# Optimization experiments

Hardware: AMD Instinct MI355X
Metric: run time of the kernel (lower is better)

Reference implementation:

```python
import jax, jax.numpy as jnp
import numpy as np

BN_EPS = 1e-5
LEAKY_SLOPE = 0.01

def setup_inputs() -> dict:
    key = jax.random.key(0)
    ks = jax.random.split(key, 8)
    B, N, C, D = 8, 2048, 128, 32  # batch, points, inchannels, outchannels
    s = 0.05
    return {
        "x": jax.random.normal(ks[0], (B, N, C), dtype=jnp.float32),
        "Wq": jax.random.normal(ks[1], (D, C), dtype=jnp.float32) * s,
        "Wk": jax.random.normal(ks[2], (D, C), dtype=jnp.float32) * s,
        "Wv": jax.random.normal(ks[3], (C, C), dtype=jnp.float32) * s,
        "Wp": jax.random.normal(ks[4], (C, C), dtype=jnp.float32) * s,
        "bn_gamma": jnp.ones((C,), dtype=jnp.float32),
        "bn_beta": jnp.zeros((C,), dtype=jnp.float32),
        "bn_mean": jax.random.normal(ks[5], (C,), dtype=jnp.float32) * 0.01,
        "bn_var": jnp.abs(jax.random.normal(ks[6], (C,), dtype=jnp.float32)) * 0.1 + 0.9,
    }

def reference(x, Wq, Wk, Wv, Wp, bn_gamma, bn_beta, bn_mean, bn_var):
    # x: [B, N, C]; 1x1 Conv1d == per-point linear map
    q = jnp.einsum('bnc,dc->bnd', x, Wq)          # [B, N, D]
    k = jnp.einsum('bnc,dc->bnd', x, Wk)          # [B, N, D]
    v = jnp.einsum('bnc,oc->bno', x, Wv)          # [B, N, C]
    energy = jnp.einsum('bnd,bmd->bnm', q, k)     # [B, Nq, Nk]
    # offset-attention: softmax over the QUERY axis (dim=1), then L1-renorm over keys
    attn = jax.nn.softmax(energy, axis=1)
    attn = attn / (1e-9 + attn.sum(axis=-1, keepdims=True))
    x_r = jnp.einsum('bnm,bmc->bnc', attn, v)     # [B, N, C]
    # project(x - x_r): 1x1 conv + BatchNorm (eval, running stats) + LeakyReLU; dropout p=0
    d = x - x_r
    y = jnp.einsum('bnc,oc->bno', d, Wp)
    y = (y - bn_mean) * (bn_gamma / jnp.sqrt(bn_var + BN_EPS)) + bn_beta
    y = jnp.where(y >= 0, y, LEAKY_SLOPE * y)
    return y + x
```

## Files before the change

### kernel.cpp

```cpp
#include <hip/hip_runtime.h>
#include <stdint.h>

#define BB 8
#define NN 2048
#define CC 128
#define DD 32
#define LOG2E 1.44269504088896340736f

typedef __attribute__((ext_vector_type(8))) short short8;
typedef __attribute__((ext_vector_type(4))) short short4v;
typedef __attribute__((ext_vector_type(4))) float f32x4;

#define MFMA(a,b,c) __builtin_amdgcn_mfma_f32_16x16x32_bf16(a,b,c,0,0,0)

__device__ __forceinline__ short f2b(float f){
  uint32_t u = __float_as_uint(f);
  uint32_t r = (u + 0x7fffu + ((u >> 16) & 1u)) >> 16;
  return (short)r;
}
__device__ __forceinline__ float b2f(short s){
  uint32_t u = ((uint32_t)(uint16_t)s) << 16;
  return __uint_as_float(u);
}

__global__ void k_pack(const float* __restrict__ Wq, const float* __restrict__ Wk,
                       const float* __restrict__ Wv, const float* __restrict__ Wp,
                       const float* __restrict__ g, const float* __restrict__ bt,
                       const float* __restrict__ mu, const float* __restrict__ vr,
                       short* __restrict__ wqkv, short* __restrict__ wp,
                       float* __restrict__ scale, float* __restrict__ shift){
  int i = blockIdx.x*256 + threadIdx.x;
  if (i < 192*128){
    int r = i >> 7, c = i & 127;
    float w = (r < 32) ? Wq[r*128+c] : (r < 64) ? Wk[(r-32)*128+c] : Wv[(r-64)*128+c];
    wqkv[i] = f2b(w);
  }
  if (i < 128*128) wp[i] = f2b(Wp[i]);
  if (i < 128){
    float s = g[i] * rsqrtf(vr[i] + 1e-5f);
    scale[i] = s;
    shift[i] = bt[i] - mu[i]*s;
  }
}

__global__ __launch_bounds__(256,4) void k_qkv(const float* __restrict__ x, const short* __restrict__ wqkv,
    short* __restrict__ qb, short* __restrict__ kb, short* __restrict__ vt){
  const int tid = threadIdx.x;
  const int wv = tid >> 6, l = tid & 63, lrow = l & 15, lg = l >> 4;
  const int r0 = blockIdx.x*16;
  const int base = wv*3;
  const float* xr = x + (long)(r0 + lrow)*CC;
  short8 a[4];
  #pragma unroll
  for (int ks=0; ks<4; ks++){
    f32x4 u0 = *(const f32x4*)(xr + ks*32 + lg*8);
    f32x4 u1 = *(const f32x4*)(xr + ks*32 + lg*8 + 4);
    short8 t;
    #pragma unroll
    for (int j=0;j<4;j++){ t[j] = f2b(u0[j]); t[4+j] = f2b(u1[j]); }
    a[ks] = t;
  }
  f32x4 acc[3];
  #pragma unroll
  for (int i=0;i<3;i++) acc[i] = f32x4{0.f,0.f,0.f,0.f};
  #pragma unroll
  for (int of=0; of<3; of++){
    #pragma unroll
    for (int ks=0; ks<4; ks++){
      short8 bfr = *(const short8*)(wqkv + ((base+of)*16 + lrow)*CC + ks*32 + lg*8);
      acc[of] = MFMA(a[ks], bfr, acc[of]);
    }
  }
  const int b = r0 / NN, nin = r0 % NN;
  #pragma unroll
  for (int of=0; of<3; of++){
    const int oo = base + of;
    const int o = oo*16 + lrow;
    if (oo < 2){
      #pragma unroll
      for (int rr=0; rr<4; rr++) qb[(long)(r0 + lg*4 + rr)*DD + o] = f2b(acc[of][rr]*LOG2E);
    } else if (oo < 4){
      #pragma unroll
      for (int rr=0; rr<4; rr++) kb[(long)(r0 + lg*4 + rr)*DD + (o-32)] = f2b(acc[of][rr]);
    } else {
      short4v s;
      #pragma unroll
      for (int rr=0; rr<4; rr++) s[rr] = f2b(acc[of][rr]);
      *(short4v*)(vt + (long)(b*CC + (o-64))*NN + nin + lg*4) = s;
    }
  }
}

__global__ __launch_bounds__(256,4) void k_colsum(const short* __restrict__ qb, const short* __restrict__ kb,
                                                  float* __restrict__ csum){
  const int tid = threadIdx.x;
  const int wv = tid >> 6, l = tid & 63, lrow = l & 15, lg = l >> 4;
  const int bq = blockIdx.x & 31;
  const int b = bq >> 2, q = bq & 3;
  const int m0 = (blockIdx.x >> 5)*64 + wv*16;
  short8 afr = *(const short8*)(kb + (long)(b*NN + m0 + lrow)*DD + lg*8);
  const short* qbase = qb + (long)b*NN*DD;
  float sum[4] = {0.f,0.f,0.f,0.f};
  f32x4 z = {0.f,0.f,0.f,0.f};
  const int nbeg = q*512, nend = nbeg + 512;
  #pragma unroll 4
  for (int n0=nbeg; n0<nend; n0+=16){
    short8 bfr = *(const short8*)(qbase + (long)(n0 + lrow)*DD + lg*8);
    f32x4 e = MFMA(afr, bfr, z);
    #pragma unroll
    for (int r=0;r<4;r++) sum[r] += exp2f(e[r]);
  }
  #pragma unroll
  for (int mask=1; mask<16; mask<<=1){
    #pragma unroll
    for (int r=0;r<4;r++) sum[r] += __shfl_xor(sum[r], mask);
  }
  if (lrow == 0){
    #pragma unroll
    for (int r=0;r<4;r++) csum[q*(BB*NN) + b*NN + m0 + lg*4 + r] = sum[r];
  }
}

__global__ __launch_bounds__(256,4) void k_attn(const short* __restrict__ qb,
    const short* __restrict__ kb, const short* __restrict__ vt, const float* __restrict__ csum,
    short* __restrict__ accPb, float* __restrict__ Lp){
  __shared__ __align__(16) short lds[17408];
  const int tid = threadIdx.x;
  const int wv = tid >> 6, l = tid & 63, lrow = l & 15, lg = l >> 4;
  const int bq = blockIdx.x & 31;
  const int b = bq >> 2;
  const int quarter = bq & 3;
  const int rt = blockIdx.x >> 5;
  const int n0 = rt*64 + wv*16;
  short8 qfr = *(const short8*)(qb + (long)(b*NN + n0 + lrow)*DD + lg*8);
  const short* kbb = kb + (long)b*NN*DD;
  const short* vtb = vt + (long)b*CC*NN;
  float* sinvl = (float*)(lds + 16384);

  const int mbase = quarter*512;
  {
    const float* c0 = csum + b*NN + mbase;
    #pragma unroll
    for (int i=tid; i<512; i+=256){
      float s = c0[i] + c0[i + BB*NN] + c0[i + 2*BB*NN] + c0[i + 3*BB*NN];
      sinvl[i] = __builtin_amdgcn_rcpf(s);
    }
  }

  f32x4 acc[8];
  #pragma unroll
  for (int i=0;i<8;i++) acc[i] = f32x4{0.f,0.f,0.f,0.f};
  float L[4] = {0.f,0.f,0.f,0.f};

  short8 sv[4]; short8 sk[2];
  const int cr = tid >> 1, hf = tid & 1;

  auto loadT = [&](int m0){
    const short* s = vtb + (long)cr*NN + m0 + hf*32;
    sv[0] = *(const short8*)(s);
    sv[1] = *(const short8*)(s+8);
    sv[2] = *(const short8*)(s+16);
    sv[3] = *(const short8*)(s+24);
    if (tid < 128){
      const short* s2 = kbb + (long)(m0 + cr)*DD + hf*16;
      sk[0] = *(const short8*)(s2);
      sk[1] = *(const short8*)(s2+8);
    }
  };
  auto storeT = [&](){
    short* vt_t = lds;
    *(short8*)(vt_t + cr*72 + hf*32 + 0)  = sv[0];
    *(short8*)(vt_t + cr*72 + hf*32 + 8)  = sv[1];
    *(short8*)(vt_t + cr*72 + hf*32 + 16) = sv[2];
    *(short8*)(vt_t + cr*72 + hf*32 + 24) = sv[3];
    if (tid < 128){
      short* kb_t = vt_t + 9216;
      *(short8*)(kb_t + cr*40 + hf*16 + 0) = sk[0];
      *(short8*)(kb_t + cr*40 + hf*16 + 8) = sk[1];
    }
  };

  loadT(mbase);
  storeT();
  __syncthreads();

  short* pl = lds + 11776 + wv*1152;
  f32x4 z = {0.f,0.f,0.f,0.f};
  for (int it=0; it<8; it++){
    const int m0 = mbase + it*64;
    if (it < 7) loadT(m0 + 64);
    short* vt_t = lds;
    short* kb_t = lds + 9216;
    float p[16];
    #pragma unroll
    for (int mt=0; mt<4; mt++){
      short8 bfr = *(short8*)(kb_t + (mt*16 + lrow)*40 + lg*8);
      f32x4 e = MFMA(qfr, bfr, z);
      float si = sinvl[it*64 + mt*16 + lrow];
      #pragma unroll
      for (int r=0;r<4;r++) p[mt*4+r] = exp2f(e[r]) * si;
    }
    #pragma unroll
    for (int r=0;r<4;r++) L[r] += (p[r] + p[4+r]) + (p[8+r] + p[12+r]);
    #pragma unroll
    for (int mt=0; mt<4; mt++){
      #pragma unroll
      for (int r=0;r<4;r++)
        pl[(lg*4+r)*72 + mt*16 + lrow] = f2b(p[mt*4+r]);
    }
    __builtin_amdgcn_s_setprio(1);
    #pragma unroll
    for (int ks=0; ks<2; ks++){
      short8 pa = *(short8*)(pl + lrow*72 + ks*32 + lg*8);
      #pragma unroll
      for (int cf=0; cf<8; cf++){
        short8 vb_ = *(short8*)(vt_t + (cf*16 + lrow)*72 + ks*32 + lg*8);
        acc[cf] = MFMA(pa, vb_, acc[cf]);
      }
    }
    __builtin_amdgcn_s_setprio(0);
    __syncthreads();
    if (it < 7){
      storeT();
      __syncthreads();
    }
  }

  #pragma unroll
  for (int mask=1; mask<16; mask<<=1){
    #pragma unroll
    for (int r=0;r<4;r++) L[r] += __shfl_xor(L[r], mask);
  }

  const long tile = (long)((b*32 + rt)*4 + quarter);
  short* aP = accPb + tile*64*128;
  #pragma unroll
  for (int cf=0; cf<8; cf++){
    #pragma unroll
    for (int r=0;r<4;r++)
      aP[(wv*16 + lg*4 + r)*128 + cf*16 + lrow] = f2b(acc[cf][r]);
  }
  if (lrow == 0){
    #pragma unroll
    for (int r=0;r<4;r++) Lp[tile*64 + wv*16 + lg*4 + r] = L[r];
  }
}

__global__ __launch_bounds__(256,4) void k_fin(const float* __restrict__ x, const short* __restrict__ accPb,
    const float* __restrict__ Lp, const short* __restrict__ wp, const float* __restrict__ scale,
    const float* __restrict__ shift, float* __restrict__ out){
  __shared__ __align__(16) short dl[16*136];
  __shared__ float linv_s[16];
  const int tid = threadIdx.x;
  const int wv = tid >> 6, l = tid & 63, lrow = l & 15, lg = l >> 4;
  const int b = blockIdx.x >> 7;
  const int rt = blockIdx.x & 127;
  const int nb = rt*16;
  const long tileIdx = (long)(b*32 + (rt>>2))*4;
  const int rowoff = (rt&3)*16;

  if (tid < 16){
    float Ls = Lp[(tileIdx+0)*64 + rowoff + tid] + Lp[(tileIdx+1)*64 + rowoff + tid]
             + Lp[(tileIdx+2)*64 + rowoff + tid] + Lp[(tileIdx+3)*64 + rowoff + tid];
    linv_s[tid] = __builtin_amdgcn_rcpf(1e-9f + Ls);
  }

  const int row_l = tid >> 4;
  const int c0 = (tid & 15)*8;
  float a[8];
  #pragma unroll
  for (int j=0;j<8;j++) a[j] = 0.f;
  #pragma unroll
  for (int p=0;p<4;p++){
    short8 v = *(const short8*)(accPb + (tileIdx+p)*64*128 + (rowoff+row_l)*128 + c0);
    #pragma unroll
    for (int j=0;j<8;j++) a[j] += b2f(v[j]);
  }
  const float* xr = x + ((long)(b*NN + nb + row_l))*CC + c0;
  f32x4 x0 = *(const f32x4*)(xr);
  f32x4 x1 = *(const f32x4*)(xr + 4);
  __syncthreads();
  {
    const float li = linv_s[row_l];
    short4v d0, d1;
    #pragma unroll
    for (int j=0;j<4;j++){
      d0[j] = f2b(x0[j] - a[j]*li);
      d1[j] = f2b(x1[j] - a[4+j]*li);
    }
    *(short4v*)(dl + row_l*136 + c0) = d0;
    *(short4v*)(dl + row_l*136 + c0 + 4) = d1;
  }
  __syncthreads();

  f32x4 yac[2];
  yac[0] = f32x4{0.f,0.f,0.f,0.f};
  yac[1] = f32x4{0.f,0.f,0.f,0.f};
  #pragma unroll
  for (int ks=0; ks<4; ks++){
    short8 da = *(short8*)(dl + lrow*136 + ks*32 + lg*8);
    #pragma unroll
    for (int of=0; of<2; of++){
      short8 wfr = *(const short8*)(wp + ((wv*2+of)*16 + lrow)*CC + ks*32 + lg*8);
      yac[of] = MFMA(da, wfr, yac[of]);
    }
  }
  float* ob = out + ((long)(b*NN + nb))*CC;
  const float* xb = x + ((long)(b*NN + nb))*CC;
  #pragma unroll
  for (int of=0; of<2; of++){
    const int o = (wv*2+of)*16 + lrow;
    const float sc = scale[o], sh = shift[o];
    #pragma unroll
    for (int r=0;r<4;r++){
      float y = yac[of][r]*sc + sh;
      y = (y >= 0.f) ? y : 0.01f*y;
      ob[(lg*4+r)*CC + o] = y + xb[(lg*4+r)*CC + o];
    }
  }
}

__global__ __launch_bounds__(256) void k_attn_mono(const float* __restrict__ x, const short* __restrict__ qb,
    const short* __restrict__ kb, const short* __restrict__ vt, const float* __restrict__ csum,
    const short* __restrict__ wp, const float* __restrict__ scale, const float* __restrict__ shift,
    float* __restrict__ out){
  __shared__ __align__(16) short lds[28160];
  const int tid = threadIdx.x;
  const int wv = tid >> 6, l = tid & 63, lrow = l & 15, lg = l >> 4;
  const int b = blockIdx.x >> 5;
  const int n0 = (blockIdx.x & 31)*64 + wv*16;
  short8 qfr = *(const short8*)(qb + (long)(b*NN + n0 + lrow)*DD + lg*8);
  const short* kbb = kb + (long)b*NN*DD;
  const short* vtb = vt + (long)b*CC*NN;
  const float* c0 = csum + b*NN;

  f32x4 acc[8];
  #pragma unroll
  for (int i=0;i<8;i++) acc[i] = f32x4{0.f,0.f,0.f,0.f};
  float L[4] = {0.f,0.f,0.f,0.f};
  short8 sv[4]; short8 sk[2];
  const int cr = tid >> 1, hf = tid & 1;
  auto loadT = [&](int m0){
    const short* s = vtb + (long)cr*NN + m0 + hf*32;
    sv[0] = *(const short8*)(s); sv[1] = *(const short8*)(s+8);
    sv[2] = *(const short8*)(s+16); sv[3] = *(const short8*)(s+24);
    if (tid < 128){
      const short* s2 = kbb + (long)(m0 + cr)*DD + hf*16;
      sk[0] = *(const short8*)(s2); sk[1] = *(const short8*)(s2+8);
    }
  };
  auto storeT = [&](int buf){
    short* vt_t = lds + buf*11776;
    *(short8*)(vt_t + cr*72 + hf*32 + 0)  = sv[0];
    *(short8*)(vt_t + cr*72 + hf*32 + 8)  = sv[1];
    *(short8*)(vt_t + cr*72 + hf*32 + 16) = sv[2];
    *(short8*)(vt_t + cr*72 + hf*32 + 24) = sv[3];
    if (tid < 128){
      short* kb_t = vt_t + 9216;
      *(short8*)(kb_t + cr*40 + hf*16 + 0) = sk[0];
      *(short8*)(kb_t + cr*40 + hf*16 + 8) = sk[1];
    }
  };
  loadT(0); storeT(0); __syncthreads();
  short* pl = lds + 23552 + wv*1152;
  f32x4 z = {0.f,0.f,0.f,0.f};
  for (int it=0; it<32; it++){
    const int m0 = it*64;
    const int cur = it & 1;
    if (it < 31) loadT(m0 + 64);
    short* vt_t = lds + cur*11776;
    short* kb_t = vt_t + 9216;
    float p[16];
    #pragma unroll
    for (int mt=0; mt<4; mt++){
      short8 bfr = *(short8*)(kb_t + (mt*16 + lrow)*40 + lg*8);
      f32x4 e = MFMA(qfr, bfr, z);
      const int m = m0 + mt*16 + lrow;
      float si = __builtin_amdgcn_rcpf(c0[m] + c0[m+BB*NN] + c0[m+2*BB*NN] + c0[m+3*BB*NN]);
      #pragma unroll
      for (int r=0;r<4;r++) p[mt*4+r] = exp2f(e[r]) * si;
    }
    #pragma unroll
    for (int r=0;r<4;r++) L[r] += (p[r] + p[4+r]) + (p[8+r] + p[12+r]);
    #pragma unroll
    for (int mt=0; mt<4; mt++){
      #pragma unroll
      for (int r=0;r<4;r++)
        pl[(lg*4+r)*72 + mt*16 + lrow] = f2b(p[mt*4+r]);
    }
    #pragma unroll
    for (int ks=0; ks<2; ks++){
      short8 pa = *(short8*)(pl + lrow*72 + ks*32 + lg*8);
      #pragma unroll
      for (int cf=0; cf<8; cf++){
        short8 vb_ = *(short8*)(vt_t + (cf*16 + lrow)*72 + ks*32 + lg*8);
        acc[cf] = MFMA(pa, vb_, acc[cf]);
      }
    }
    if (it < 31) storeT((it+1) & 1);
    __syncthreads();
  }
  #pragma unroll
  for (int mask=1; mask<16; mask<<=1){
    #pragma unroll
    for (int r=0;r<4;r++) L[r] += __shfl_xor(L[r], mask);
  }
  float linv[4];
  #pragma unroll
  for (int r=0;r<4;r++) linv[r] = __builtin_amdgcn_rcpf(1e-9f + L[r]);
  const float* xbb = x + (long)(b*NN + n0)*CC;
  float xv[32];
  short* dl = lds + wv*2176;
  #pragma unroll
  for (int cf=0; cf<8; cf++){
    #pragma unroll
    for (int r=0;r<4;r++){
      float xx = xbb[(lg*4+r)*CC + cf*16 + lrow];
      xv[cf*4+r] = xx;
      dl[(lg*4+r)*136 + cf*16 + lrow] = f2b(xx - acc[cf][r]*linv[r]);
    }
  }
  f32x4 yac[8];
  #pragma unroll
  for (int i=0;i<8;i++) yac[i] = f32x4{0.f,0.f,0.f,0.f};
  #pragma unroll
  for (int ks=0; ks<4; ks++){
    short8 da = *(short8*)(dl + lrow*136 + ks*32 + lg*8);
    #pragma unroll
    for (int of=0; of<8; of++){
      short8 wfr = *(const short8*)(wp + (of*16 + lrow)*CC + ks*32 + lg*8);
      yac[of] = MFMA(da, wfr, yac[of]);
    }
  }
  float* ob = out + (long)(b*NN + n0)*CC;
  #pragma unroll
  for (int of=0; of<8; of++){
    const int o = of*16 + lrow;
    const float sc = scale[o], sh = shift[o];
    #pragma unroll
    for (int r=0;r<4;r++){
      float y = yac[of][r]*sc + sh;
      y = (y >= 0.f) ? y : 0.01f*y;
      ob[(lg*4+r)*CC + o] = y + xv[of*4+r];
    }
  }
}

extern "C" void kernel_launch(void* const* d_in, const int* in_sizes, int n_in,
                              void* d_out, int out_size, void* d_ws, size_t ws_size,
                              hipStream_t stream) {
  const float* x  = (const float*)d_in[0];
  const float* Wq = (const float*)d_in[1];
  const float* Wk = (const float*)d_in[2];
  const float* Wv = (const float*)d_in[3];
  const float* Wp = (const float*)d_in[4];
  const float* g  = (const float*)d_in[5];
  const float* bt = (const float*)d_in[6];
  const float* mu = (const float*)d_in[7];
  const float* vr = (const float*)d_in[8];
  float* out = (float*)d_out;

  char* ws = (char*)d_ws;
  short* wqkv  = (short*)(ws + 0);
  short* wp    = (short*)(ws + 49152);
  float* scale = (float*)(ws + 81920);
  float* shift = (float*)(ws + 82432);
  short* qb    = (short*)(ws + 98304);
  short* kb    = (short*)(ws + 1146880);
  short* vt    = (short*)(ws + 2195456);
  float* csum  = (float*)(ws + 6389760);
  float* Lp    = (float*)(ws + 6651904);
  short* accPb = (short*)(ws + 6914048);
  const size_t need_split = 6914048 + 16777216;

  k_pack<<<96, 256, 0, stream>>>(Wq, Wk, Wv, Wp, g, bt, mu, vr, wqkv, wp, scale, shift);
  k_qkv<<<1024, 256, 0, stream>>>(x, wqkv, qb, kb, vt);
  k_colsum<<<1024, 256, 0, stream>>>(qb, kb, csum);
  if (ws_size >= need_split){
    k_attn<<<1024, 256, 0, stream>>>(qb, kb, vt, csum, accPb, Lp);
    k_fin<<<1024, 256, 0, stream>>>(x, accPb, Lp, wp, scale, shift, out);
  } else {
    k_attn_mono<<<256, 256, 0, stream>>>(x, qb, kb, vt, csum, wp, scale, shift, out);
  }
}
```

Baseline: 131.2 us.

## Split attention key dimension across waves and drop weight packing kernel

The attention kernel now gives each wave a 16-key slice, and every wave handles all 64 query rows. Each wave computes transposed energy with K as the A operand, so the probabilities feed straight into 16x16x16 MFMAs against V without a round trip through LDS. Partial accumulators from the four waves are then reduced through LDS in bf16 before being written out. This drops the per-wave P staging, but it raises register pressure (launch bounds go to 2 blocks per SIMD) and adds an extra bf16 rounding step. Separately, the k_pack kernel is removed, with the weights converted to bf16 and the BN scale/shift computed inline in k_qkv and k_fin. The mono fallback path is also deleted.

```diff
diff --git a/kernel.cpp b/kernel.cpp
--- a/kernel.cpp
+++ b/kernel.cpp
@@ -13,6 +13,17 @@
 
 #define MFMA(a,b,c) __builtin_amdgcn_mfma_f32_16x16x32_bf16(a,b,c,0,0,0)
 
+__device__ __forceinline__ f32x4 MFMA16(short4v a, short4v b, f32x4 c){
+#if __has_builtin(__builtin_amdgcn_mfma_f32_16x16x16bf16_1k)
+  return __builtin_amdgcn_mfma_f32_16x16x16bf16_1k(a, b, c, 0, 0, 0);
+#else
+  f32x4 d;
+  asm volatile("s_nop 1\n\tv_mfma_f32_16x16x16_bf16 %0, %1, %2, %3\n\ts_nop 4"
+               : "=&v"(d) : "v"(a), "v"(b), "v"(c));
+  return d;
+#endif
+}
+
 __device__ __forceinline__ short f2b(float f){
   uint32_t u = __float_as_uint(f);
   uint32_t r = (u + 0x7fffu + ((u >> 16) & 1u)) >> 16;
@@ -23,27 +34,8 @@
   return __uint_as_float(u);
 }
 
-__global__ void k_pack(const float* __restrict__ Wq, const float* __restrict__ Wk,
-                       const float* __restrict__ Wv, const float* __restrict__ Wp,
-                       const float* __restrict__ g, const float* __restrict__ bt,
-                       const float* __restrict__ mu, const float* __restrict__ vr,
-                       short* __restrict__ wqkv, short* __restrict__ wp,
-                       float* __restrict__ scale, float* __restrict__ shift){
-  int i = blockIdx.x*256 + threadIdx.x;
-  if (i < 192*128){
-    int r = i >> 7, c = i & 127;
-    float w = (r < 32) ? Wq[r*128+c] : (r < 64) ? Wk[(r-32)*128+c] : Wv[(r-64)*128+c];
-    wqkv[i] = f2b(w);
-  }
-  if (i < 128*128) wp[i] = f2b(Wp[i]);
-  if (i < 128){
-    float s = g[i] * rsqrtf(vr[i] + 1e-5f);
-    scale[i] = s;
-    shift[i] = bt[i] - mu[i]*s;
-  }
-}
-
-__global__ __launch_bounds__(256,4) void k_qkv(const float* __restrict__ x, const short* __restrict__ wqkv,
+__global__ __launch_bounds__(256,4) void k_qkv(const float* __restrict__ x,
+    const float* __restrict__ Wq, const float* __restrict__ Wk, const float* __restrict__ Wv,
     short* __restrict__ qb, short* __restrict__ kb, short* __restrict__ vt){
   const int tid = threadIdx.x;
   const int wv = tid >> 6, l = tid & 63, lrow = l & 15, lg = l >> 4;
@@ -65,9 +57,16 @@
   for (int i=0;i<3;i++) acc[i] = f32x4{0.f,0.f,0.f,0.f};
   #pragma unroll
   for (int of=0; of<3; of++){
+    const int oo = base + of;
+    const int row = oo*16 + lrow;
+    const float* Wr = (oo < 2) ? (Wq + row*CC) : (oo < 4) ? (Wk + (row-32)*CC) : (Wv + (row-64)*CC);
     #pragma unroll
     for (int ks=0; ks<4; ks++){
-      short8 bfr = *(const short8*)(wqkv + ((base+of)*16 + lrow)*CC + ks*32 + lg*8);
+      f32x4 w0 = *(const f32x4*)(Wr + ks*32 + lg*8);
+      f32x4 w1 = *(const f32x4*)(Wr + ks*32 + lg*8 + 4);
+      short8 bfr;
+      #pragma unroll
+      for (int j=0;j<4;j++){ bfr[j] = f2b(w0[j]); bfr[4+j] = f2b(w1[j]); }
       acc[of] = MFMA(a[ks], bfr, acc[of]);
     }
   }
@@ -121,40 +120,45 @@
   }
 }
 
-__global__ __launch_bounds__(256,4) void k_attn(const short* __restrict__ qb,
+__global__ __launch_bounds__(256,2) void k_attn(const short* __restrict__ qb,
     const short* __restrict__ kb, const short* __restrict__ vt, const float* __restrict__ csum,
     short* __restrict__ accPb, float* __restrict__ Lp){
-  __shared__ __align__(16) short lds[17408];
+  __shared__ __align__(16) short lds[16896];
   const int tid = threadIdx.x;
-  const int wv = tid >> 6, l = tid & 63, lrow = l & 15, lg = l >> 4;
+  const int kw = tid >> 6, l = tid & 63, lrow = l & 15, lg = l >> 4;
   const int bq = blockIdx.x & 31;
   const int b = bq >> 2;
   const int quarter = bq & 3;
   const int rt = blockIdx.x >> 5;
-  const int n0 = rt*64 + wv*16;
-  short8 qfr = *(const short8*)(qb + (long)(b*NN + n0 + lrow)*DD + lg*8);
+  const int n0 = rt*64;
   const short* kbb = kb + (long)b*NN*DD;
   const short* vtb = vt + (long)b*CC*NN;
-  float* sinvl = (float*)(lds + 16384);
+  float* sinvl = (float*)(lds + 11776);
+
+  short8 qfr[4];
+  #pragma unroll
+  for (int rg=0; rg<4; rg++)
+    qfr[rg] = *(const short8*)(qb + (long)(b*NN + n0 + rg*16 + lrow)*DD + lg*8);
 
   const int mbase = quarter*512;
   {
-    const float* c0 = csum + b*NN + mbase;
+    const float* c0p = csum + b*NN + mbase;
     #pragma unroll
     for (int i=tid; i<512; i+=256){
-      float s = c0[i] + c0[i + BB*NN] + c0[i + 2*BB*NN] + c0[i + 3*BB*NN];
+      float s = c0p[i] + c0p[i + BB*NN] + c0p[i + 2*BB*NN] + c0p[i + 3*BB*NN];
       sinvl[i] = __builtin_amdgcn_rcpf(s);
     }
   }
 
-  f32x4 acc[8];
-  #pragma unroll
-  for (int i=0;i<8;i++) acc[i] = f32x4{0.f,0.f,0.f,0.f};
-  float L[4] = {0.f,0.f,0.f,0.f};
+  f32x4 acc[4][8];
+  #pragma unroll
+  for (int rg=0; rg<4; rg++)
+    #pragma unroll
+    for (int i=0;i<8;i++) acc[rg][i] = f32x4{0.f,0.f,0.f,0.f};
+  float Lacc[4] = {0.f,0.f,0.f,0.f};
 
   short8 sv[4]; short8 sk[2];
   const int cr = tid >> 1, hf = tid & 1;
-
   auto loadT = [&](int m0){
     const short* s = vtb + (long)cr*NN + m0 + hf*32;
     sv[0] = *(const short8*)(s);
@@ -168,13 +172,12 @@
     }
   };
   auto storeT = [&](){
-    short* vt_t = lds;
-    *(short8*)(vt_t + cr*72 + hf*32 + 0)  = sv[0];
-    *(short8*)(vt_t + cr*72 + hf*32 + 8)  = sv[1];
-    *(short8*)(vt_t + cr*72 + hf*32 + 16) = sv[2];
-    *(short8*)(vt_t + cr*72 + hf*32 + 24) = sv[3];
+    *(short8*)(lds + cr*72 + hf*32 + 0)  = sv[0];
+    *(short8*)(lds + cr*72 + hf*32 + 8)  = sv[1];
+    *(short8*)(lds + cr*72 + hf*32 + 16) = sv[2];
+    *(short8*)(lds + cr*72 + hf*32 + 24) = sv[3];
     if (tid < 128){
-      short* kb_t = vt_t + 9216;
+      short* kb_t = lds + 9216;
       *(short8*)(kb_t + cr*40 + hf*16 + 0) = sk[0];
       *(short8*)(kb_t + cr*40 + hf*16 + 8) = sk[1];
     }
@@ -184,39 +187,28 @@
   storeT();
   __syncthreads();
 
-  short* pl = lds + 11776 + wv*1152;
   f32x4 z = {0.f,0.f,0.f,0.f};
   for (int it=0; it<8; it++){
-    const int m0 = mbase + it*64;
-    if (it < 7) loadT(m0 + 64);
-    short* vt_t = lds;
-    short* kb_t = lds + 9216;
-    float p[16];
-    #pragma unroll
-    for (int mt=0; mt<4; mt++){
-      short8 bfr = *(short8*)(kb_t + (mt*16 + lrow)*40 + lg*8);
-      f32x4 e = MFMA(qfr, bfr, z);
-      float si = sinvl[it*64 + mt*16 + lrow];
-      #pragma unroll
-      for (int r=0;r<4;r++) p[mt*4+r] = exp2f(e[r]) * si;
-    }
-    #pragma unroll
-    for (int r=0;r<4;r++) L[r] += (p[r] + p[4+r]) + (p[8+r] + p[12+r]);
-    #pragma unroll
-    for (int mt=0; mt<4; mt++){
-      #pragma unroll
-      for (int r=0;r<4;r++)
-        pl[(lg*4+r)*72 + mt*16 + lrow] = f2b(p[mt*4+r]);
-    }
+    if (it < 7) loadT(mbase + it*64 + 64);
+    short8 kfr = *(short8*)(lds + 9216 + (kw*16 + lrow)*40 + lg*8);
+    float si[4];
+    #pragma unroll
+    for (int r=0;r<4;r++) si[r] = sinvl[it*64 + kw*16 + lg*4 + r];
+    short4v vbf[8];
+    #pragma unroll
+    for (int cf=0; cf<8; cf++)
+      vbf[cf] = *(short4v*)(lds + (cf*16 + lrow)*72 + kw*16 + lg*4);
     __builtin_amdgcn_s_setprio(1);
     #pragma unroll
-    for (int ks=0; ks<2; ks++){
-      short8 pa = *(short8*)(pl + lrow*72 + ks*32 + lg*8);
-      #pragma unroll
-      for (int cf=0; cf<8; cf++){
-        short8 vb_ = *(short8*)(vt_t + (cf*16 + lrow)*72 + ks*32 + lg*8);
-        acc[cf] = MFMA(pa, vb_, acc[cf]);
-      }
+    for (int rg=0; rg<4; rg++){
+      f32x4 e = MFMA(kfr, qfr[rg], z);
+      float p0 = exp2f(e[0])*si[0], p1 = exp2f(e[1])*si[1];
+      float p2 = exp2f(e[2])*si[2], p3 = exp2f(e[3])*si[3];
+      Lacc[rg] += (p0+p1) + (p2+p3);
+      short4v pa; pa[0]=f2b(p0); pa[1]=f2b(p1); pa[2]=f2b(p2); pa[3]=f2b(p3);
+      #pragma unroll
+      for (int cf=0; cf<8; cf++)
+        acc[rg][cf] = MFMA16(pa, vbf[cf], acc[rg][cf]);
     }
     __builtin_amdgcn_s_setprio(0);
     __syncthreads();
@@ -226,29 +218,70 @@
     }
   }
 
-  #pragma unroll
-  for (int mask=1; mask<16; mask<<=1){
-    #pragma unroll
-    for (int r=0;r<4;r++) L[r] += __shfl_xor(L[r], mask);
-  }
-
   const long tile = (long)((b*32 + rt)*4 + quarter);
-  short* aP = accPb + tile*64*128;
-  #pragma unroll
-  for (int cf=0; cf<8; cf++){
-    #pragma unroll
-    for (int r=0;r<4;r++)
-      aP[(wv*16 + lg*4 + r)*128 + cf*16 + lrow] = f2b(acc[cf][r]);
-  }
-  if (lrow == 0){
-    #pragma unroll
-    for (int r=0;r<4;r++) Lp[tile*64 + wv*16 + lg*4 + r] = L[r];
+
+  float Lr[4];
+  #pragma unroll
+  for (int rg=0; rg<4; rg++){
+    float v = Lacc[rg];
+    v += __shfl_xor(v, 16);
+    v += __shfl_xor(v, 32);
+    Lr[rg] = v;
+  }
+  float* Lb = (float*)(lds + 16384);
+  if (l < 16){
+    #pragma unroll
+    for (int rg=0; rg<4; rg++) Lb[kw*64 + rg*16 + l] = Lr[rg];
+  }
+  __syncthreads();
+  if (l < 16){
+    float s = Lb[kw*16 + l] + Lb[64 + kw*16 + l] + Lb[128 + kw*16 + l] + Lb[192 + kw*16 + l];
+    Lp[tile*64 + kw*16 + l] = s;
+  }
+
+  for (int round=0; round<2; round++){
+    const int c0 = round*2;
+    #pragma unroll
+    for (int cc=0; cc<2; cc++){
+      short* dst = lds + (cc*4 + kw)*2048;
+      const int c = c0 + cc;
+      #pragma unroll
+      for (int cf=0; cf<8; cf++)
+        #pragma unroll
+        for (int r=0;r<4;r++)
+          dst[(lg*4+r)*128 + cf*16 + lrow] = f2b(acc[c][cf][r]);
+    }
+    __syncthreads();
+    {
+      const int cc = kw & 1;
+      const int row = (kw>>1)*8 + (l>>3);
+      const int cb = (l&7)*16;
+      const short* src = lds + cc*8192 + row*128 + cb;
+      float s[16];
+      #pragma unroll
+      for (int j=0;j<16;j++) s[j] = 0.f;
+      #pragma unroll
+      for (int slot=0; slot<4; slot++){
+        short8 v0 = *(const short8*)(src + slot*2048);
+        short8 v1 = *(const short8*)(src + slot*2048 + 8);
+        #pragma unroll
+        for (int j=0;j<8;j++){ s[j] += b2f(v0[j]); s[8+j] += b2f(v1[j]); }
+      }
+      short8 o0, o1;
+      #pragma unroll
+      for (int j=0;j<8;j++){ o0[j] = f2b(s[j]); o1[j] = f2b(s[8+j]); }
+      short* aP = accPb + tile*64*128 + ((c0+cc)*16 + row)*128 + cb;
+      *(short8*)aP = o0;
+      *(short8*)(aP + 8) = o1;
+    }
+    __syncthreads();
   }
 }
 
 __global__ __launch_bounds__(256,4) void k_fin(const float* __restrict__ x, const short* __restrict__ accPb,
-    const float* __restrict__ Lp, const short* __restrict__ wp, const float* __restrict__ scale,
-    const float* __restrict__ shift, float* __restrict__ out){
+    const float* __restrict__ Lp, const float* __restrict__ Wp, const float* __restrict__ g,
+    const float* __restrict__ bt, const float* __restrict__ mu, const float* __restrict__ vr,
+    float* __restrict__ out){
   __shared__ __align__(16) short dl[16*136];
   __shared__ float linv_s[16];
   const int tid = threadIdx.x;
@@ -301,7 +334,12 @@
     short8 da = *(short8*)(dl + lrow*136 + ks*32 + lg*8);
     #pragma unroll
     for (int of=0; of<2; of++){
-      short8 wfr = *(const short8*)(wp + ((wv*2+of)*16 + lrow)*CC + ks*32 + lg*8);
+      const float* wr = Wp + ((wv*2+of)*16 + lrow)*CC + ks*32 + lg*8;
+      f32x4 w0 = *(const f32x4*)(wr);
+      f32x4 w1 = *(const f32x4*)(wr + 4);
+      short8 wfr;
+      #pragma unroll
+      for (int j=0;j<4;j++){ wfr[j] = f2b(w0[j]); wfr[4+j] = f2b(w1[j]); }
       yac[of] = MFMA(da, wfr, yac[of]);
     }
   }
@@ -310,138 +348,13 @@
   #pragma unroll
   for (int of=0; of<2; of++){
     const int o = (wv*2+of)*16 + lrow;
-    const float sc = scale[o], sh = shift[o];
+    const float sc = g[o] * rsqrtf(vr[o] + 1e-5f);
+    const float sh = bt[o] - mu[o]*sc;
     #pragma unroll
     for (int r=0;r<4;r++){
       float y = yac[of][r]*sc + sh;
       y = (y >= 0.f) ? y : 0.01f*y;
       ob[(lg*4+r)*CC + o] = y + xb[(lg*4+r)*CC + o];
-    }
-  }
-}
-
-__global__ __launch_bounds__(256) void k_attn_mono(const float* __restrict__ x, const short* __restrict__ qb,
-    const short* __restrict__ kb, const short* __restrict__ vt, const float* __restrict__ csum,
-    const short* __restrict__ wp, const float* __restrict__ scale, const float* __restrict__ shift,
-    float* __restrict__ out){
-  __shared__ __align__(16) short lds[28160];
-  const int tid = threadIdx.x;
-  const int wv = tid >> 6, l = tid & 63, lrow = l & 15, lg = l >> 4;
-  const int b = blockIdx.x >> 5;
-  const int n0 = (blockIdx.x & 31)*64 + wv*16;
-  short8 qfr = *(const short8*)(qb + (long)(b*NN + n0 + lrow)*DD + lg*8);
-  const short* kbb = kb + (long)b*NN*DD;
-  const short* vtb = vt + (long)b*CC*NN;
-  const float* c0 = csum + b*NN;
-
-  f32x4 acc[8];
-  #pragma unroll
-  for (int i=0;i<8;i++) acc[i] = f32x4{0.f,0.f,0.f,0.f};
-  float L[4] = {0.f,0.f,0.f,0.f};
-  short8 sv[4]; short8 sk[2];
-  const int cr = tid >> 1, hf = tid & 1;
-  auto loadT = [&](int m0){
-    const short* s = vtb + (long)cr*NN + m0 + hf*32;
-    sv[0] = *(const short8*)(s); sv[1] = *(const short8*)(s+8);
-    sv[2] = *(const short8*)(s+16); sv[3] = *(const short8*)(s+24);
-    if (tid < 128){
-      const short* s2 = kbb + (long)(m0 + cr)*DD + hf*16;
-      sk[0] = *(const short8*)(s2); sk[1] = *(const short8*)(s2+8);
-    }
-  };
-  auto storeT = [&](int buf){
-    short* vt_t = lds + buf*11776;
-    *(short8*)(vt_t + cr*72 + hf*32 + 0)  = sv[0];
-    *(short8*)(vt_t + cr*72 + hf*32 + 8)  = sv[1];
-    *(short8*)(vt_t + cr*72 + hf*32 + 16) = sv[2];
-    *(short8*)(vt_t + cr*72 + hf*32 + 24) = sv[3];
-    if (tid < 128){
-      short* kb_t = vt_t + 9216;
-      *(short8*)(kb_t + cr*40 + hf*16 + 0) = sk[0];
-      *(short8*)(kb_t + cr*40 + hf*16 + 8) = sk[1];
-    }
-  };
-  loadT(0); storeT(0); __syncthreads();
-  short* pl = lds + 23552 + wv*1152;
-  f32x4 z = {0.f,0.f,0.f,0.f};
-  for (int it=0; it<32; it++){
-    const int m0 = it*64;
-    const int cur = it & 1;
-    if (it < 31) loadT(m0 + 64);
-    short* vt_t = lds + cur*11776;
-    short* kb_t = vt_t + 9216;
-    float p[16];
-    #pragma unroll
-    for (int mt=0; mt<4; mt++){
-      short8 bfr = *(short8*)(kb_t + (mt*16 + lrow)*40 + lg*8);
-      f32x4 e = MFMA(qfr, bfr, z);
-      const int m = m0 + mt*16 + lrow;
-      float si = __builtin_amdgcn_rcpf(c0[m] + c0[m+BB*NN] + c0[m+2*BB*NN] + c0[m+3*BB*NN]);
-      #pragma unroll
-      for (int r=0;r<4;r++) p[mt*4+r] = exp2f(e[r]) * si;
-    }
-    #pragma unroll
-    for (int r=0;r<4;r++) L[r] += (p[r] + p[4+r]) + (p[8+r] + p[12+r]);
-    #pragma unroll
-    for (int mt=0; mt<4; mt++){
-      #pragma unroll
-      for (int r=0;r<4;r++)
-        pl[(lg*4+r)*72 + mt*16 + lrow] = f2b(p[mt*4+r]);
-    }
-    #pragma unroll
-    for (int ks=0; ks<2; ks++){
-      short8 pa = *(short8*)(pl + lrow*72 + ks*32 + lg*8);
-      #pragma unroll
-      for (int cf=0; cf<8; cf++){
-        short8 vb_ = *(short8*)(vt_t + (cf*16 + lrow)*72 + ks*32 + lg*8);
-        acc[cf] = MFMA(pa, vb_, acc[cf]);
-      }
-    }
-    if (it < 31) storeT((it+1) & 1);
-    __syncthreads();
-  }
-  #pragma unroll
-  for (int mask=1; mask<16; mask<<=1){
-    #pragma unroll
-    for (int r=0;r<4;r++) L[r] += __shfl_xor(L[r], mask);
-  }
-  float linv[4];
-  #pragma unroll
-  for (int r=0;r<4;r++) linv[r] = __builtin_amdgcn_rcpf(1e-9f + L[r]);
-  const float* xbb = x + (long)(b*NN + n0)*CC;
-  float xv[32];
-  short* dl = lds + wv*2176;
-  #pragma unroll
-  for (int cf=0; cf<8; cf++){
-    #pragma unroll
-    for (int r=0;r<4;r++){
-      float xx = xbb[(lg*4+r)*CC + cf*16 + lrow];
-      xv[cf*4+r] = xx;
-      dl[(lg*4+r)*136 + cf*16 + lrow] = f2b(xx - acc[cf][r]*linv[r]);
-    }
-  }
-  f32x4 yac[8];
-  #pragma unroll
-  for (int i=0;i<8;i++) yac[i] = f32x4{0.f,0.f,0.f,0.f};
-  #pragma unroll
-  for (int ks=0; ks<4; ks++){
-    short8 da = *(short8*)(dl + lrow*136 + ks*32 + lg*8);
-    #pragma unroll
-    for (int of=0; of<8; of++){
-      short8 wfr = *(const short8*)(wp + (of*16 + lrow)*CC + ks*32 + lg*8);
-      yac[of] = MFMA(da, wfr, yac[of]);
-    }
-  }
-  float* ob = out + (long)(b*NN + n0)*CC;
-  #pragma unroll
-  for (int of=0; of<8; of++){
-    const int o = of*16 + lrow;
-    const float sc = scale[o], sh = shift[o];
-    #pragma unroll
-    for (int r=0;r<4;r++){
-      float y = yac[of][r]*sc + sh;
-      y = (y >= 0.f) ? y : 0.01f*y;
-      ob[(lg*4+r)*CC + o] = y + xv[of*4+r];
     }
   }
 }
@@ -461,25 +374,15 @@
   float* out = (float*)d_out;
 
   char* ws = (char*)d_ws;
-  short* wqkv  = (short*)(ws + 0);
-  short* wp    = (short*)(ws + 49152);
-  float* scale = (float*)(ws + 81920);
-  float* shift = (float*)(ws + 82432);
   short* qb    = (short*)(ws + 98304);
   short* kb    = (short*)(ws + 1146880);
   short* vt    = (short*)(ws + 2195456);
   float* csum  = (float*)(ws + 6389760);
   float* Lp    = (float*)(ws + 6651904);
   short* accPb = (short*)(ws + 6914048);
-  const size_t need_split = 6914048 + 16777216;
-
-  k_pack<<<96, 256, 0, stream>>>(Wq, Wk, Wv, Wp, g, bt, mu, vr, wqkv, wp, scale, shift);
-  k_qkv<<<1024, 256, 0, stream>>>(x, wqkv, qb, kb, vt);
+
+  k_qkv<<<1024, 256, 0, stream>>>(x, Wq, Wk, Wv, qb, kb, vt);
   k_colsum<<<1024, 256, 0, stream>>>(qb, kb, csum);
-  if (ws_size >= need_split){
-    k_attn<<<1024, 256, 0, stream>>>(qb, kb, vt, csum, accPb, Lp);
-    k_fin<<<1024, 256, 0, stream>>>(x, accPb, Lp, wp, scale, shift, out);
-  } else {
-    k_attn_mono<<<256, 256, 0, stream>>>(x, qb, kb, vt, csum, wp, scale, shift, out);
-  }
-}
+  k_attn<<<1024, 256, 0, stream>>>(qb, kb, vt, csum, accPb, Lp);
+  k_fin<<<1024, 256, 0, stream>>>(x, accPb, Lp, Wp, g, bt, mu, vr, out);
+}
```

Result: slower. 145.4 us (+10.9%).
